# Performance work log

Hardware: AMD Instinct MI355X
Metric: run time of the kernel (lower is better)

The kernel has to match this reference:

```python
import jax, jax.numpy as jnp
import numpy as np

HIDDEN = 1024
HEADS = 16
HEAD_DIM = HIDDEN // HEADS
POS_DIM = 128
B, S = 2, 2048
ROPE_BASE = 10000.0


def setup_inputs() -> dict:
    key = jax.random.key(0)
    ks = jax.random.split(key, 8)
    sd = 1.0 / np.sqrt(HIDDEN)
    return {
        "x":   jax.random.normal(ks[0], (B, S, HIDDEN), dtype=jnp.float32),
        "W_q": jax.random.normal(ks[1], (HIDDEN, HIDDEN), dtype=jnp.float32) * sd,
        "W_k": jax.random.normal(ks[2], (HIDDEN, HIDDEN), dtype=jnp.float32) * sd,
        "W_v": jax.random.normal(ks[3], (HIDDEN, HIDDEN), dtype=jnp.float32) * sd,
        "W_o": jax.random.normal(ks[4], (HIDDEN, HIDDEN), dtype=jnp.float32) * sd,
        "repo_W1": jax.random.normal(ks[5], (HIDDEN, POS_DIM), dtype=jnp.float32) * sd,
        "repo_b1": jnp.zeros((POS_DIM,), dtype=jnp.float32),
        "repo_W2": jax.random.normal(ks[6], (POS_DIM, 1), dtype=jnp.float32) * (1.0 / np.sqrt(POS_DIM)),
        "repo_b2": jnp.zeros((1,), dtype=jnp.float32),
    }


def _repo_positions(x, W1, b1, W2, b2):
    # 2-layer MLP -> scalar per token; softplus + cumsum gives monotone learned positions
    h = jax.nn.gelu(jnp.einsum("bsd,dp->bsp", x, W1) + b1)
    raw = (jnp.einsum("bsp,po->bso", h, W2) + b2)[..., 0]      # (B, S)
    return jnp.cumsum(jax.nn.softplus(raw), axis=1)             # (B, S)


def _apply_rope(q, k, positions):
    # q, k: (B, S, H, Dh); positions: (B, S) continuous
    half = HEAD_DIM // 2
    inv_freq = 1.0 / (ROPE_BASE ** (jnp.arange(0, HEAD_DIM, 2, dtype=jnp.float32) / HEAD_DIM))
    angles = positions[:, :, None] * inv_freq                   # (B, S, half)
    cos = jnp.cos(angles)[:, :, None, :]                        # (B, S, 1, half)
    sin = jnp.sin(angles)[:, :, None, :]

    def rot(t):
        t1, t2 = t[..., :half], t[..., half:]
        return jnp.concatenate([t1 * cos - t2 * sin, t1 * sin + t2 * cos], axis=-1)

    return rot(q), rot(k)


def reference(x, W_q, W_k, W_v, W_o, repo_W1, repo_b1, repo_W2, repo_b2):
    scale = 1.0 / np.sqrt(HEAD_DIM)
    q = jnp.einsum("bsd,de->bse", x, W_q).reshape(B, S, HEADS, HEAD_DIM)
    k = jnp.einsum("bsd,de->bse", x, W_k).reshape(B, S, HEADS, HEAD_DIM)
    v = jnp.einsum("bsd,de->bse", x, W_v).reshape(B, S, HEADS, HEAD_DIM)

    positions = _repo_positions(x, repo_W1, repo_b1, repo_W2, repo_b2)
    q, k = _apply_rope(q, k, positions)

    # explicit O(S^2) attention, matching the torch module
    scores = jnp.einsum("bqhd,bkhd->bhqk", q, k) * scale        # (B, H, S, S)
    attn = jax.nn.softmax(scores, axis=-1)
    out = jnp.einsum("bhqk,bkhd->bqhd", attn, v)                # (B, S, H, Dh)
    out = out.reshape(B, S, HIDDEN)
    return jnp.einsum("bsd,de->bse", out, W_o)
```

## Files before the change

### kernel.cpp

```cpp
#include <hip/hip_runtime.h>
#include <hip/hip_bf16.h>
#include <math.h>

#define HIDDEN 1024
#define HEADS 16
#define HEAD_DIM 64
#define POS_DIM 128
#define BATCH 2
#define SEQ 2048
#define TOKENS (BATCH * SEQ)

typedef _Float16 f16;
typedef __attribute__((ext_vector_type(8))) _Float16 f16x8;
typedef __attribute__((ext_vector_type(4))) _Float16 f16x4;
typedef __attribute__((ext_vector_type(4))) float f32x4;

__device__ __forceinline__ void glds16(const f16* g, f16* l) {
    __builtin_amdgcn_global_load_lds((const __attribute__((address_space(1))) unsigned int*)g,
                                     (__attribute__((address_space(3))) unsigned int*)l, 16, 0, 0);
}

__global__ __launch_bounds__(256) void cast_x_kernel(const float* __restrict__ x,
                                                     f16* __restrict__ o) {
    const int i = (blockIdx.x * 256 + threadIdx.x) * 8;
    const float4 u = *(const float4*)(x + i);
    const float4 v = *(const float4*)(x + i + 4);
    f16x8 r = {(f16)u.x, (f16)u.y, (f16)u.z, (f16)u.w,
               (f16)v.x, (f16)v.y, (f16)v.z, (f16)v.w};
    *(f16x8*)(o + i) = r;
}

__global__ __launch_bounds__(256) void cast_wt4_kernel(const float* __restrict__ W0,
                                                       const float* __restrict__ W1,
                                                       const float* __restrict__ W2,
                                                       const float* __restrict__ W3,
                                                       f16* __restrict__ Wt) {
    __shared__ float ts[32][33];
    const int t = threadIdx.x;
    const int z = blockIdx.z;
    const float* W = (z == 0) ? W0 : (z == 1) ? W1 : (z == 2) ? W2 : W3;
    f16* dst = Wt + (size_t)z * HIDDEN * HIDDEN;
    const int k0 = blockIdx.y * 32, n0 = blockIdx.x * 32;
    {
        const int r = t >> 3, c4 = (t & 7) * 4;
        const float4 u = *(const float4*)(W + (size_t)(k0 + r) * HIDDEN + n0 + c4);
        ts[r][c4 + 0] = u.x; ts[r][c4 + 1] = u.y; ts[r][c4 + 2] = u.z; ts[r][c4 + 3] = u.w;
    }
    __syncthreads();
    {
        const int r = t >> 3, c4 = (t & 7) * 4;
        f16* o = dst + (size_t)(n0 + r) * HIDDEN + k0 + c4;
        o[0] = (f16)ts[c4 + 0][r]; o[1] = (f16)ts[c4 + 1][r];
        o[2] = (f16)ts[c4 + 2][r]; o[3] = (f16)ts[c4 + 3][r];
    }
}

__global__ __launch_bounds__(256) void cast_w1t_kernel(const float* __restrict__ W1,
                                                       f16* __restrict__ Wh,
                                                       f16* __restrict__ Wl) {
    __shared__ float ts[32][33];
    const int t = threadIdx.x;
    const int k0 = blockIdx.y * 32, p0 = blockIdx.x * 32;
    {
        const int r = t >> 3, c4 = (t & 7) * 4;
        const float4 u = *(const float4*)(W1 + (size_t)(k0 + r) * POS_DIM + p0 + c4);
        ts[r][c4 + 0] = u.x; ts[r][c4 + 1] = u.y; ts[r][c4 + 2] = u.z; ts[r][c4 + 3] = u.w;
    }
    __syncthreads();
    {
        const int r = t >> 3, c4 = (t & 7) * 4;
        f16* oh = Wh + (size_t)(p0 + r) * HIDDEN + k0 + c4;
        f16* ol = Wl + (size_t)(p0 + r) * HIDDEN + k0 + c4;
#pragma unroll
        for (int u = 0; u < 4; ++u) {
            const float v = ts[c4 + u][r];
            const f16 hi = (f16)v;
            oh[u] = hi;
            ol[u] = (f16)(v - (float)hi);
        }
    }
}

__global__ __launch_bounds__(256, 3) void gemm_gll(const f16* __restrict__ A,
                                                   const f16* __restrict__ Bt,
                                                   f16* __restrict__ Cb,
                                                   float* __restrict__ Cf,
                                                   int N, int f16out) {
    __shared__ __align__(16) f16 As[128 * 64];
    __shared__ __align__(16) f16 Bs[128 * 64];
    const int tid = threadIdx.x;
    const int w = tid >> 6, lane = tid & 63;
    const int g = lane >> 4, c = lane & 15;
    const int m0 = blockIdx.y * 128, n0 = blockIdx.x * 128;
    const int wm = (w & 1) * 64, wn = (w >> 1) * 64;

    const int lrow = lane >> 3;
    const int lseg = (lane & 7) ^ lrow;
    const f16* gA = A + (size_t)(m0 + w * 32 + lrow) * 1024 + lseg * 8;
    const f16* gB = Bt + (size_t)(n0 + w * 32 + lrow) * 1024 + lseg * 8;
    f16* lA = &As[(w * 32) * 64];
    f16* lB = &Bs[(w * 32) * 64];

    f32x4 acc[4][4];
    const f32x4 z = {0.f, 0.f, 0.f, 0.f};
#pragma unroll
    for (int i = 0; i < 4; ++i)
#pragma unroll
        for (int j = 0; j < 4; ++j) acc[i][j] = z;

    const int rsw = c & 7;
    for (int k0 = 0; k0 < 1024; k0 += 64) {
        __syncthreads();
#pragma unroll
        for (int p = 0; p < 4; ++p) {
            glds16(gA + (size_t)p * 8 * 1024 + k0, lA + p * 8 * 64);
            glds16(gB + (size_t)p * 8 * 1024 + k0, lB + p * 8 * 64);
        }
        __syncthreads();
#pragma unroll
        for (int s = 0; s < 2; ++s) {
            f16x8 af[4], bf[4];
#pragma unroll
            for (int i = 0; i < 4; ++i)
                af[i] = *(const f16x8*)&As[(wm + i * 16 + c) * 64 + (((s * 4 + g) ^ rsw) * 8)];
#pragma unroll
            for (int j = 0; j < 4; ++j)
                bf[j] = *(const f16x8*)&Bs[(wn + j * 16 + c) * 64 + (((s * 4 + g) ^ rsw) * 8)];
#pragma unroll
            for (int i = 0; i < 4; ++i)
#pragma unroll
                for (int j = 0; j < 4; ++j)
                    acc[i][j] = __builtin_amdgcn_mfma_f32_16x16x32_f16(af[i], bf[j], acc[i][j], 0, 0, 0);
        }
    }
#pragma unroll
    for (int i = 0; i < 4; ++i)
#pragma unroll
        for (int j = 0; j < 4; ++j)
#pragma unroll
            for (int r = 0; r < 4; ++r) {
                const size_t off = (size_t)(m0 + wm + i * 16 + 4 * g + r) * N + n0 + wn + j * 16 + c;
                if (f16out) Cb[off] = (f16)acc[i][j][r];
                else Cf[off] = acc[i][j][r];
            }
}

__device__ __forceinline__ float gelu_tanh(float x) {
    const float kA = 0.7978845608028654f;
    return 0.5f * x * (1.0f + tanhf(kA * (x + 0.044715f * x * x * x)));
}

__global__ __launch_bounds__(256, 2) void repo_mfma(const float* __restrict__ x,
                                                    const f16* __restrict__ w1h,
                                                    const f16* __restrict__ w1l,
                                                    const float* __restrict__ b1,
                                                    const float* __restrict__ W2,
                                                    const float* __restrict__ b2,
                                                    float* __restrict__ raw) {
    __shared__ __align__(16) f16 Ash[64 * 32], Asl[64 * 32];
    __shared__ __align__(16) f16 Bsh[128 * 32], Bsl[128 * 32];
    __shared__ float red[4][64];
    const int tid = threadIdx.x;
    const int w = tid >> 6, lane = tid & 63;
    const int g = lane >> 4, c = lane & 15;
    const int m0 = blockIdx.x * 64;

    const int arow = tid >> 2, aseg = tid & 3;
    const int aslot = (aseg ^ ((arow ^ (arow >> 2)) & 3)) << 3;
    const float* gA = x + (size_t)(m0 + arow) * 1024 + aseg * 8;
    const f16* gBh0 = w1h + (size_t)arow * 1024 + aseg * 8;
    const f16* gBh1 = w1h + (size_t)(arow + 64) * 1024 + aseg * 8;
    const f16* gBl0 = w1l + (size_t)arow * 1024 + aseg * 8;
    const f16* gBl1 = w1l + (size_t)(arow + 64) * 1024 + aseg * 8;
    f16* sAh = &Ash[arow * 32 + aslot];
    f16* sAl = &Asl[arow * 32 + aslot];
    f16* sBh0 = &Bsh[arow * 32 + aslot];
    f16* sBh1 = &Bsh[(arow + 64) * 32 + aslot];
    f16* sBl0 = &Bsl[arow * 32 + aslot];
    f16* sBl1 = &Bsl[(arow + 64) * 32 + aslot];

    const int foff = ((g ^ ((c ^ (c >> 2)) & 3)) << 3);

    f32x4 acc[4][2];
    const f32x4 z = {0.f, 0.f, 0.f, 0.f};
#pragma unroll
    for (int i = 0; i < 4; ++i) { acc[i][0] = z; acc[i][1] = z; }

    float4 pa0 = *(const float4*)gA;
    float4 pa1 = *(const float4*)(gA + 4);
    f16x8 pbh0 = *(const f16x8*)gBh0, pbh1 = *(const f16x8*)gBh1;
    f16x8 pbl0 = *(const f16x8*)gBl0, pbl1 = *(const f16x8*)gBl1;

    for (int k0 = 0; k0 < 1024; k0 += 32) {
        __syncthreads();
        {
            const float av[8] = {pa0.x, pa0.y, pa0.z, pa0.w, pa1.x, pa1.y, pa1.z, pa1.w};
            f16x8 ah, al;
#pragma unroll
            for (int u = 0; u < 8; ++u) {
                const f16 hi = (f16)av[u];
                ah[u] = hi;
                al[u] = (f16)(av[u] - (float)hi);
            }
            *(f16x8*)sAh = ah; *(f16x8*)sAl = al;
            *(f16x8*)sBh0 = pbh0; *(f16x8*)sBh1 = pbh1;
            *(f16x8*)sBl0 = pbl0; *(f16x8*)sBl1 = pbl1;
        }
        __syncthreads();
        if (k0 + 32 < 1024) {
            pa0 = *(const float4*)(gA + k0 + 32);
            pa1 = *(const float4*)(gA + k0 + 36);
            pbh0 = *(const f16x8*)(gBh0 + k0 + 32);
            pbh1 = *(const f16x8*)(gBh1 + k0 + 32);
            pbl0 = *(const f16x8*)(gBl0 + k0 + 32);
            pbl1 = *(const f16x8*)(gBl1 + k0 + 32);
        }
        f16x8 ah[4], al[4], bh[2], bl[2];
#pragma unroll
        for (int i = 0; i < 4; ++i) {
            ah[i] = *(const f16x8*)&Ash[(i * 16 + c) * 32 + foff];
            al[i] = *(const f16x8*)&Asl[(i * 16 + c) * 32 + foff];
        }
#pragma unroll
        for (int j = 0; j < 2; ++j) {
            bh[j] = *(const f16x8*)&Bsh[(w * 32 + j * 16 + c) * 32 + foff];
            bl[j] = *(const f16x8*)&Bsl[(w * 32 + j * 16 + c) * 32 + foff];
        }
#pragma unroll
        for (int i = 0; i < 4; ++i)
#pragma unroll
            for (int j = 0; j < 2; ++j) {
                acc[i][j] = __builtin_amdgcn_mfma_f32_16x16x32_f16(ah[i], bh[j], acc[i][j], 0, 0, 0);
                acc[i][j] = __builtin_amdgcn_mfma_f32_16x16x32_f16(ah[i], bl[j], acc[i][j], 0, 0, 0);
                acc[i][j] = __builtin_amdgcn_mfma_f32_16x16x32_f16(al[i], bh[j], acc[i][j], 0, 0, 0);
            }
    }
    float b1v[2], w2v[2];
#pragma unroll
    for (int j = 0; j < 2; ++j) {
        const int col = w * 32 + j * 16 + c;
        b1v[j] = b1[col];
        w2v[j] = W2[col];
    }
    float part[4][4];
#pragma unroll
    for (int i = 0; i < 4; ++i)
#pragma unroll
        for (int r = 0; r < 4; ++r) {
            float s = 0.f;
#pragma unroll
            for (int j = 0; j < 2; ++j)
                s += gelu_tanh(acc[i][j][r] + b1v[j]) * w2v[j];
            s += __shfl_xor(s, 1, 64);
            s += __shfl_xor(s, 2, 64);
            s += __shfl_xor(s, 4, 64);
            s += __shfl_xor(s, 8, 64);
            part[i][r] = s;
        }
    if (c == 0)
#pragma unroll
        for (int i = 0; i < 4; ++i)
#pragma unroll
            for (int r = 0; r < 4; ++r)
                red[w][i * 16 + 4 * g + r] = part[i][r];
    __syncthreads();
    if (tid < 64)
        raw[m0 + tid] = red[0][tid] + red[1][tid] + red[2][tid] + red[3][tid] + b2[0];
}

__device__ __forceinline__ double softplus_d(double x) {
    return (x > 0.0) ? x + log1p(exp(-x)) : log1p(exp(x));
}

__global__ __launch_bounds__(256) void repo_cumsum_kernel(const float* __restrict__ raw,
                                                          float* __restrict__ pos) {
    __shared__ double bufA[256];
    __shared__ double bufB[256];
    const int b = blockIdx.x;
    const int t = threadIdx.x;
    const float* r = raw + (size_t)b * SEQ;

    double loc[8];
    double sum = 0.0;
#pragma unroll
    for (int i = 0; i < 8; ++i) {
        sum += softplus_d((double)r[t * 8 + i]);
        loc[i] = sum;
    }
    bufA[t] = sum;
    __syncthreads();

    double* src = bufA;
    double* dst = bufB;
    for (int off = 1; off < 256; off <<= 1) {
        double v = src[t];
        if (t >= off) v += src[t - off];
        dst[t] = v;
        __syncthreads();
        double* tmp = src; src = dst; dst = tmp;
    }
    const double excl = src[t] - sum;
#pragma unroll
    for (int i = 0; i < 8; ++i)
        pos[(size_t)b * SEQ + t * 8 + i] = (float)(excl + loc[i]);
}

__global__ __launch_bounds__(256) void sctab_kernel(const float* __restrict__ pos,
                                                    float* __restrict__ costab,
                                                    float* __restrict__ sintab) {
    const int idx = blockIdx.x * 256 + threadIdx.x;
    const int tok = idx >> 5, i = idx & 31;
    const double ang = (double)pos[tok] * exp(-(double)i * 0.28782313662425574);
    double sa, ca;
    sincos(ang, &sa, &ca);
    costab[idx] = (float)ca;
    sintab[idx] = (float)sa;
}

__global__ __launch_bounds__(256) void packkv_kernel(f16* __restrict__ qkv,
                                                     const float* __restrict__ costab,
                                                     const float* __restrict__ sintab,
                                                     f16* __restrict__ kfo,
                                                     f16* __restrict__ vfo) {
    __shared__ __align__(16) f16 kds[64][72];
    __shared__ __align__(16) f16 vds[64][72];
    const int t = threadIdx.x;
    const int s0 = blockIdx.x * 64;
    const int h = blockIdx.y, b = blockIdx.z;
    const int key = t >> 2, part = t & 3;
    const int tok = b * SEQ + s0 + key;
    {
        float cs[8], sn[8];
        *(float4*)cs       = *(const float4*)(costab + tok * 32 + part * 8);
        *(float4*)(cs + 4) = *(const float4*)(costab + tok * 32 + part * 8 + 4);
        *(float4*)sn       = *(const float4*)(sintab + tok * 32 + part * 8);
        *(float4*)(sn + 4) = *(const float4*)(sintab + tok * 32 + part * 8 + 4);
        f16* qrow = qkv + (size_t)tok * 3072 + h * HEAD_DIM;
        {
            f16x8 lo = *(const f16x8*)(qrow + part * 8);
            f16x8 hi = *(const f16x8*)(qrow + part * 8 + 32);
#pragma unroll
            for (int u = 0; u < 8; ++u) {
                const float l = (float)lo[u], hh = (float)hi[u];
                lo[u] = (f16)(l * cs[u] - hh * sn[u]);
                hi[u] = (f16)(l * sn[u] + hh * cs[u]);
            }
            *(f16x8*)(qrow + part * 8) = lo;
            *(f16x8*)(qrow + part * 8 + 32) = hi;
        }
        const f16* krow = qrow + 1024;
        {
            f16x8 lo = *(const f16x8*)(krow + part * 8);
            f16x8 hi = *(const f16x8*)(krow + part * 8 + 32);
#pragma unroll
            for (int u = 0; u < 8; ++u) {
                const float l = (float)lo[u], hh = (float)hi[u];
                kds[key][part * 8 + u]      = (f16)(l * cs[u] - hh * sn[u]);
                kds[key][32 + part * 8 + u] = (f16)(l * sn[u] + hh * cs[u]);
            }
        }
        const f16* vrow = qrow + 2048;
        f16x8 v0 = *(const f16x8*)(vrow + part * 16);
        f16x8 v1 = *(const f16x8*)(vrow + part * 16 + 8);
#pragma unroll
        for (int u = 0; u < 8; ++u) {
            vds[part * 16 + u][key] = v0[u];
            vds[part * 16 + 8 + u][key] = v1[u];
        }
    }
    __syncthreads();
    const size_t cb = ((size_t)((b * HEADS + h) * 32) + blockIdx.x) * 4096;
#pragma unroll
    for (int p = 0; p < 2; ++p) {
        const int idx = p * 256 + t;
        const int frag = idx >> 6, lane = idx & 63;
        const int jn = frag >> 1, half = frag & 1, g = lane >> 4, c = lane & 15;
        *(f16x8*)(kfo + cb + frag * 512 + lane * 8) =
            *(const f16x8*)(&kds[jn * 16 + c][half * 32 + g * 8]);
    }
#pragma unroll
    for (int p = 0; p < 4; ++p) {
        const int idx = p * 256 + t;
        const int frag = idx >> 6, lane = idx & 63;
        const int jd = frag >> 2, jn = frag & 3, g = lane >> 4, c = lane & 15;
        *(f16x4*)(vfo + cb + frag * 256 + lane * 4) =
            *(const f16x4*)(&vds[jd * 16 + c][jn * 16 + 4 * g]);
    }
}

__global__ __launch_bounds__(256, 2) void attn_f16(const f16* __restrict__ qkv,
                                                   const f16* __restrict__ kfr,
                                                   const f16* __restrict__ vfr,
                                                   f16* __restrict__ aof0,
                                                   f16* __restrict__ aof1,
                                                   float* __restrict__ lsb) {
    __shared__ __align__(16) f16 ot[4][32][72];
    const int tid = threadIdx.x;
    const int w = tid >> 6, lane = tid & 63;
    const int g = lane >> 4, c = lane & 15;
    const int h = blockIdx.y;
    const int b = blockIdx.z >> 1, half = blockIdx.z & 1;
    const int bh = b * HEADS + h;
    const int row0 = blockIdx.x * 128 + w * 32;
    const int ch0 = half * 16;

    const f16* qb = qkv + (size_t)(b * SEQ + row0) * 3072 + h * HEAD_DIM + g * 8;
    const f16* kfb = kfr + (size_t)bh * 32 * 4096;
    const f16* vfb = vfr + (size_t)bh * 32 * 4096;

    f16x8 qf[2][2];
#pragma unroll
    for (int i = 0; i < 2; ++i) {
        qf[i][0] = *(const f16x8*)(qb + (size_t)(i * 16 + c) * 3072);
        qf[i][1] = *(const f16x8*)(qb + (size_t)(i * 16 + c) * 3072 + 32);
    }
    const f32x4 z = {0.f, 0.f, 0.f, 0.f};
    f32x4 acc[4][2];
    f32x4 accl[2];
#pragma unroll
    for (int jd = 0; jd < 4; ++jd) { acc[jd][0] = z; acc[jd][1] = z; }
    accl[0] = z; accl[1] = z;

    const f16x4 ones = {(f16)1.f, (f16)1.f, (f16)1.f, (f16)1.f};
    const float SC = 0.125f * 1.4426950408889634f;

    auto loadfr = [&](int ch, f16x8* kf, f16x4* vf) {
        const f16* kp = kfb + (size_t)ch * 4096 + lane * 8;
#pragma unroll
        for (int f = 0; f < 8; ++f) kf[f] = *(const f16x8*)(kp + f * 512);
        const f16* vp = vfb + (size_t)ch * 4096 + lane * 4;
#pragma unroll
        for (int f = 0; f < 16; ++f) vf[f] = *(const f16x4*)(vp + f * 256);
    };
    auto step = [&](const f16x8* kf, const f16x4* vf) {
#pragma unroll
        for (int i = 0; i < 2; ++i) {
            f32x4 s[4];
#pragma unroll
            for (int jn = 0; jn < 4; ++jn) {
                s[jn] = __builtin_amdgcn_mfma_f32_16x16x32_f16(kf[jn * 2], qf[i][0], z, 0, 0, 0);
                s[jn] = __builtin_amdgcn_mfma_f32_16x16x32_f16(kf[jn * 2 + 1], qf[i][1], s[jn], 0, 0, 0);
            }
#pragma unroll
            for (int jn = 0; jn < 4; ++jn) {
                f16x4 pf;
#pragma unroll
                for (int r = 0; r < 4; ++r)
                    pf[r] = (f16)__builtin_amdgcn_exp2f(fmaf(s[jn][r], SC, -8.0f));
                accl[i] = __builtin_amdgcn_mfma_f32_16x16x16f16(ones, pf, accl[i], 0, 0, 0);
#pragma unroll
                for (int jd = 0; jd < 4; ++jd)
                    acc[jd][i] = __builtin_amdgcn_mfma_f32_16x16x16f16(vf[jd * 4 + jn], pf, acc[jd][i], 0, 0, 0);
            }
        }
    };

    f16x8 kA[8], kB[8];
    f16x4 vA[16], vB[16];
    loadfr(ch0, kA, vA);
    for (int ch = 0; ch < 16; ch += 2) {
        loadfr(ch0 + ch + 1, kB, vB);
        step(kA, vA);
        loadfr(ch0 + ((ch + 2) & 15), kA, vA);
        step(kB, vB);
    }

    if (lane < 16) {
#pragma unroll
        for (int i = 0; i < 2; ++i)
            lsb[((size_t)(half * 32 + bh)) * SEQ + row0 + i * 16 + lane] = accl[i][0];
    }
#pragma unroll
    for (int i = 0; i < 2; ++i)
#pragma unroll
        for (int jd = 0; jd < 4; ++jd)
#pragma unroll
            for (int r = 0; r < 4; ++r)
                ot[w][i * 16 + c][jd * 16 + 4 * g + r] = (f16)acc[jd][i][r];
    f16* aofH = half ? aof1 : aof0;
    const int tr = lane >> 1, hf = lane & 1;
    f16* aob = aofH + (size_t)(b * SEQ + row0 + tr) * HIDDEN + h * HEAD_DIM + hf * 32;
#pragma unroll
    for (int q = 0; q < 4; ++q)
        *(f16x8*)(aob + q * 8) = *(const f16x8*)(&ot[w][tr][hf * 32 + q * 8]);
}

__global__ __launch_bounds__(256) void combine_kernel(f16* __restrict__ a0,
                                                      const f16* __restrict__ a1,
                                                      const float* __restrict__ lsb) {
    const int idx = blockIdx.x * 256 + threadIdx.x;
    const int part = idx & 127;
    const int tok = idx >> 7;
    const int h = part >> 3, d8 = (part & 7) * 8;
    const int b = tok >> 11, s = tok & 2047;
    const size_t li = (size_t)(b * HEADS + h) * SEQ + s;
    const float inv = 1.0f / (lsb[li] + lsb[32 * SEQ + li]);
    const size_t off = (size_t)tok * HIDDEN + h * HEAD_DIM + d8;
    const f16x8 u = *(const f16x8*)(a0 + off);
    const f16x8 v = *(const f16x8*)(a1 + off);
    f16x8 o;
#pragma unroll
    for (int q = 0; q < 8; ++q) o[q] = (f16)(((float)u[q] + (float)v[q]) * inv);
    *(f16x8*)(a0 + off) = o;
}

extern "C" void kernel_launch(void* const* d_in, const int* in_sizes, int n_in,
                              void* d_out, int out_size, void* d_ws, size_t ws_size,
                              hipStream_t stream) {
    const float* x   = (const float*)d_in[0];
    const float* W_q = (const float*)d_in[1];
    const float* W_k = (const float*)d_in[2];
    const float* W_v = (const float*)d_in[3];
    const float* W_o = (const float*)d_in[4];
    const float* rW1 = (const float*)d_in[5];
    const float* rb1 = (const float*)d_in[6];
    const float* rW2 = (const float*)d_in[7];
    const float* rb2 = (const float*)d_in[8];
    float* out = (float*)d_out;

    const size_t MAT = (size_t)TOKENS * HIDDEN;
    const size_t WSZ = (size_t)HIDDEN * HIDDEN;
    f16* x16  = (f16*)d_ws;
    f16* wqkv = x16 + MAT;
    f16* wot  = wqkv + 3 * WSZ;
    f16* qkv  = wot + WSZ;
    f16* kfr  = qkv + 3 * MAT;
    f16* vfr  = kfr + MAT;
    f16* aof0 = vfr + MAT;
    f16* aof1 = aof0 + MAT;
    f16* w1h  = aof1 + MAT;
    f16* w1l  = w1h + POS_DIM * HIDDEN;
    float* raw    = (float*)(w1l + POS_DIM * HIDDEN);
    float* pos    = raw + TOKENS;
    float* costab = pos + TOKENS;
    float* sintab = costab + TOKENS * 32;
    float* lsb    = sintab + TOKENS * 32;

    cast_x_kernel<<<MAT / 2048, 256, 0, stream>>>(x, x16);
    cast_wt4_kernel<<<dim3(32, 32, 4), 256, 0, stream>>>(W_q, W_k, W_v, W_o, wqkv);
    cast_w1t_kernel<<<dim3(4, 32), 256, 0, stream>>>(rW1, w1h, w1l);

    gemm_gll<<<dim3(24, 32), 256, 0, stream>>>(x16, wqkv, qkv, nullptr, 3072, 1);

    repo_mfma<<<64, 256, 0, stream>>>(x, w1h, w1l, rb1, rW2, rb2, raw);
    repo_cumsum_kernel<<<BATCH, 256, 0, stream>>>(raw, pos);
    sctab_kernel<<<TOKENS * 32 / 256, 256, 0, stream>>>(pos, costab, sintab);

    packkv_kernel<<<dim3(SEQ / 64, HEADS, BATCH), 256, 0, stream>>>(qkv, costab, sintab, kfr, vfr);

    attn_f16<<<dim3(SEQ / 128, HEADS, BATCH * 2), 256, 0, stream>>>(qkv, kfr, vfr, aof0, aof1, lsb);
    combine_kernel<<<TOKENS * 128 / 256, 256, 0, stream>>>(aof0, aof1, lsb);

    gemm_gll<<<dim3(8, 32), 256, 0, stream>>>(aof0, wot, nullptr, out, 1024, 0);
}
```

Baseline: 261.8 us.

## Stage K/V chunks through LDS with global_load_lds instead of per-wave register loads

Each block now loads every K/V chunk once into shared memory using direct global-to-LDS loads split across the four waves, then each wave reads its fragments from LDS. Before, every wave fetched the same chunk from global memory into registers, with double buffering to hide latency. The change cuts redundant global/L2 traffic and register pressure. It drops the software prefetch and adds two block barriers per chunk, so load latency is no longer overlapped with MFMA work.

```diff
diff --git a/kernel.cpp b/kernel.cpp
--- a/kernel.cpp
+++ b/kernel.cpp
@@ -394,6 +394,8 @@
                                                    f16* __restrict__ aof0,
                                                    f16* __restrict__ aof1,
                                                    float* __restrict__ lsb) {
+    __shared__ __align__(16) f16 kls[4096];
+    __shared__ __align__(16) f16 vls[4096];
     __shared__ __align__(16) f16 ot[4][32][72];
     const int tid = threadIdx.x;
     const int w = tid >> 6, lane = tid & 63;
@@ -424,15 +426,26 @@
     const f16x4 ones = {(f16)1.f, (f16)1.f, (f16)1.f, (f16)1.f};
     const float SC = 0.125f * 1.4426950408889634f;
 
-    auto loadfr = [&](int ch, f16x8* kf, f16x4* vf) {
-        const f16* kp = kfb + (size_t)ch * 4096 + lane * 8;
-#pragma unroll
-        for (int f = 0; f < 8; ++f) kf[f] = *(const f16x8*)(kp + f * 512);
-        const f16* vp = vfb + (size_t)ch * 4096 + lane * 4;
-#pragma unroll
-        for (int f = 0; f < 16; ++f) vf[f] = *(const f16x4*)(vp + f * 256);
-    };
-    auto step = [&](const f16x8* kf, const f16x4* vf) {
+    for (int cc = 0; cc < 16; ++cc) {
+        const int ch = ch0 + cc;
+        __syncthreads();
+        {
+            const f16* kg = kfb + (size_t)ch * 4096 + w * 1024 + lane * 8;
+            const f16* vg = vfb + (size_t)ch * 4096 + w * 1024 + lane * 8;
+            glds16(kg, kls + w * 1024);
+            glds16(kg + 512, kls + w * 1024 + 512);
+            glds16(vg, vls + w * 1024);
+            glds16(vg + 512, vls + w * 1024 + 512);
+        }
+        __syncthreads();
+
+        f16x8 kf[8];
+        f16x4 vf[16];
+#pragma unroll
+        for (int f = 0; f < 8; ++f) kf[f] = *(const f16x8*)(kls + lane * 8 + f * 512);
+#pragma unroll
+        for (int f = 0; f < 16; ++f) vf[f] = *(const f16x4*)(vls + lane * 4 + f * 256);
+
 #pragma unroll
         for (int i = 0; i < 2; ++i) {
             f32x4 s[4];
@@ -453,16 +466,6 @@
                     acc[jd][i] = __builtin_amdgcn_mfma_f32_16x16x16f16(vf[jd * 4 + jn], pf, acc[jd][i], 0, 0, 0);
             }
         }
-    };
-
-    f16x8 kA[8], kB[8];
-    f16x4 vA[16], vB[16];
-    loadfr(ch0, kA, vA);
-    for (int ch = 0; ch < 16; ch += 2) {
-        loadfr(ch0 + ch + 1, kB, vB);
-        step(kA, vA);
-        loadfr(ch0 + ((ch + 2) & 15), kA, vA);
-        step(kB, vB);
     }
 
     if (lane < 16) {
```

Measured after the change: 250.4 us. 4.4% less time.
